# Optimization experiments

Hardware: AMD Instinct MI355X
Metric: run time of the kernel (lower is better)

The kernel has to match this reference:

```python
import jax, jax.numpy as jnp
import numpy as np

B, T, D, H, E = 4, 512, 2048, 1024, 2


def setup_inputs() -> dict:
    key = jax.random.key(0)
    k = jax.random.split(key, 4)
    return {
        "x": jax.random.normal(k[0], (B, T, D), jnp.float32),
        "Wg": jax.random.normal(k[1], (D, E), jnp.float32) / np.float32(np.sqrt(D)),
        "W1": jax.random.normal(k[2], (E, D, H), jnp.float32) / np.float32(np.sqrt(D)),
        "b1": jnp.zeros((E, H), jnp.float32),
        "W2": jax.random.normal(k[3], (E, H, D), jnp.float32) / np.float32(np.sqrt(H)),
        "b2": jnp.zeros((E, D), jnp.float32),
    }


def reference(x, Wg, W1, b1, W2, b2):
    # --- Top1 gate: bias-free linear -> softmax -> argmax routing ---
    logits = jnp.einsum('btd,de->bte', x, Wg)            # [B,T,E]
    probs = jax.nn.softmax(logits, axis=-1)
    idx = jnp.argmax(probs, axis=-1)                     # [B,T] chosen expert
    gate = jnp.max(probs, axis=-1)                       # [B,T] top-1 prob
    # --- expert FFN (identity activation): fc1 -> fc2, batched per expert ---
    h = jnp.einsum('btd,edh->ebth', x, W1) + b1[:, None, None, :]   # [E,B,T,H]
    y = jnp.einsum('ebth,ehd->ebtd', h, W2) + b2[:, None, None, :]  # [E,B,T,D]
    # --- combine: select routed expert output, scale by gate value ---
    sel = jax.nn.one_hot(idx, E, dtype=x.dtype) * gate[..., None]   # [B,T,E]
    moe_out = jnp.einsum('ebtd,bte->btd', y, sel)                   # [B,T,D]
    # --- model head: sum over model_dim, log_softmax over tokens ---
    return jax.nn.log_softmax(jnp.sum(moe_out, axis=2), axis=1)     # [B,T]
```

## Files before the change

### kernel.cpp

```cpp
#include <hip/hip_runtime.h>

#define B_ 4
#define T_ 512
#define D_ 2048
#define H_ 1024
#define E_ 2

__device__ __forceinline__ float waveReduceSum(float v) {
    #pragma unroll
    for (int o = 32; o > 0; o >>= 1) v += __shfl_down(v, o, 64);
    return v;
}

__device__ __forceinline__ float blockReduceSum256(float v, float* lds) {
    int lane = threadIdx.x & 63;
    int wid  = threadIdx.x >> 6;
    v = waveReduceSum(v);
    if (lane == 0) lds[wid] = v;
    __syncthreads();
    float r = 0.f;
    if (threadIdx.x == 0) {
        r = lds[0] + lds[1] + lds[2] + lds[3];
    }
    __syncthreads();
    return r;
}

__global__ void k_w2sum(const float* __restrict__ W2, float* __restrict__ w2s) {
    __shared__ float lds[4];
    int row = blockIdx.x;
    const float* p = W2 + (size_t)row * D_;
    float acc = 0.f;
    for (int i = threadIdx.x * 4; i < D_; i += blockDim.x * 4) {
        float4 v = *reinterpret_cast<const float4*>(p + i);
        acc += (v.x + v.y) + (v.z + v.w);
    }
    acc = blockReduceSum256(acc, lds);
    if (threadIdx.x == 0) w2s[row] = acc;
}

__global__ void k_vred(const float* __restrict__ W1, const float* __restrict__ w2s,
                       float* __restrict__ v) {
    __shared__ float lds[4];
    int row = blockIdx.x;
    int e = row / D_;
    const float* p = W1 + (size_t)row * H_;
    const float* w = w2s + e * H_;
    float acc = 0.f;
    for (int i = threadIdx.x * 4; i < H_; i += blockDim.x * 4) {
        float4 a = *reinterpret_cast<const float4*>(p + i);
        float4 b = *reinterpret_cast<const float4*>(w + i);
        acc += a.x * b.x + a.y * b.y + a.z * b.z + a.w * b.w;
    }
    acc = blockReduceSum256(acc, lds);
    if (threadIdx.x == 0) v[row] = acc;
}

__global__ void k_cbias(const float* __restrict__ b1, const float* __restrict__ w2s,
                        const float* __restrict__ b2, float* __restrict__ c) {
    __shared__ float lds[4];
    int e = blockIdx.x;
    float acc = 0.f;
    for (int i = threadIdx.x; i < H_; i += blockDim.x)
        acc += b1[e * H_ + i] * w2s[e * H_ + i];
    for (int i = threadIdx.x; i < D_; i += blockDim.x)
        acc += b2[e * D_ + i];
    acc = blockReduceSum256(acc, lds);
    if (threadIdx.x == 0) c[e] = acc;
}

__global__ void k_token(const float* __restrict__ x, const float* __restrict__ Wg,
                        const float* __restrict__ v, const float* __restrict__ c,
                        float* __restrict__ s) {
    __shared__ float lds[4][4];
    int bt = blockIdx.x;
    const float* xp = x + (size_t)bt * D_;
    float g0 = 0.f, g1 = 0.f, d0 = 0.f, d1 = 0.f;
    for (int i = threadIdx.x * 4; i < D_; i += blockDim.x * 4) {
        float4 xv   = *reinterpret_cast<const float4*>(xp + i);
        float4 v0   = *reinterpret_cast<const float4*>(v + i);
        float4 v1   = *reinterpret_cast<const float4*>(v + D_ + i);
        float4 wg01 = *reinterpret_cast<const float4*>(Wg + i * 2);
        float4 wg23 = *reinterpret_cast<const float4*>(Wg + i * 2 + 4);
        g0 += xv.x * wg01.x + xv.y * wg01.z + xv.z * wg23.x + xv.w * wg23.z;
        g1 += xv.x * wg01.y + xv.y * wg01.w + xv.z * wg23.y + xv.w * wg23.w;
        d0 += xv.x * v0.x + xv.y * v0.y + xv.z * v0.z + xv.w * v0.w;
        d1 += xv.x * v1.x + xv.y * v1.y + xv.z * v1.z + xv.w * v1.w;
    }
    #pragma unroll
    for (int o = 32; o > 0; o >>= 1) {
        g0 += __shfl_down(g0, o, 64);
        g1 += __shfl_down(g1, o, 64);
        d0 += __shfl_down(d0, o, 64);
        d1 += __shfl_down(d1, o, 64);
    }
    int lane = threadIdx.x & 63;
    int wid  = threadIdx.x >> 6;
    if (lane == 0) {
        lds[wid][0] = g0; lds[wid][1] = g1; lds[wid][2] = d0; lds[wid][3] = d1;
    }
    __syncthreads();
    if (threadIdx.x == 0) {
        float G0 = 0.f, G1 = 0.f, Dt0 = 0.f, Dt1 = 0.f;
        #pragma unroll
        for (int w = 0; w < 4; ++w) {
            G0 += lds[w][0]; G1 += lds[w][1]; Dt0 += lds[w][2]; Dt1 += lds[w][3];
        }
        int e = (G1 > G0) ? 1 : 0;
        float m  = fmaxf(G0, G1);
        float p0 = expf(G0 - m), p1 = expf(G1 - m);
        float gate = ((e == 0) ? p0 : p1) / (p0 + p1);
        float dot  = (e == 0) ? Dt0 : Dt1;
        s[bt] = gate * (dot + c[e]);
    }
}

__global__ void k_lsm(const float* __restrict__ s, float* __restrict__ out) {
    __shared__ float lds[8];
    int b = blockIdx.x;
    int t = threadIdx.x;
    int lane = t & 63, wid = t >> 6;
    float val = s[b * T_ + t];

    float m = val;
    #pragma unroll
    for (int o = 1; o < 64; o <<= 1) m = fmaxf(m, __shfl_xor(m, o, 64));
    if (lane == 0) lds[wid] = m;
    __syncthreads();
    m = lds[0];
    #pragma unroll
    for (int w = 1; w < 8; ++w) m = fmaxf(m, lds[w]);
    __syncthreads();

    float ex = expf(val - m);
    float sum = ex;
    #pragma unroll
    for (int o = 1; o < 64; o <<= 1) sum += __shfl_xor(sum, o, 64);
    if (lane == 0) lds[wid] = sum;
    __syncthreads();
    sum = 0.f;
    #pragma unroll
    for (int w = 0; w < 8; ++w) sum += lds[w];

    out[b * T_ + t] = val - m - logf(sum);
}

extern "C" void kernel_launch(void* const* d_in, const int* in_sizes, int n_in,
                              void* d_out, int out_size, void* d_ws, size_t ws_size,
                              hipStream_t stream) {
    (void)in_sizes; (void)n_in; (void)out_size; (void)ws_size;
    const float* x  = (const float*)d_in[0];
    const float* Wg = (const float*)d_in[1];
    const float* W1 = (const float*)d_in[2];
    const float* b1 = (const float*)d_in[3];
    const float* W2 = (const float*)d_in[4];
    const float* b2 = (const float*)d_in[5];
    float* out = (float*)d_out;

    float* ws  = (float*)d_ws;
    float* w2s = ws;
    float* v   = ws + 2048;
    float* c   = ws + 6144;
    float* s   = ws + 6160;

    k_w2sum<<<E_ * H_, 256, 0, stream>>>(W2, w2s);
    k_vred <<<E_ * D_, 256, 0, stream>>>(W1, w2s, v);
    k_cbias<<<E_,      256, 0, stream>>>(b1, w2s, b2, c);
    k_token<<<B_ * T_, 256, 0, stream>>>(x, Wg, v, c, s);
    k_lsm  <<<B_,      512, 0, stream>>>(s, out);
}
```

Measured before the change: 26.71 us.

## Fuse bias and log-softmax kernels, use one wave per row reductions

Each reduction kernel now assigns a whole row to a single 64-lane wave with fully unrolled float4 loads, so the block-level LDS reductions and barriers go away. The bias-constant computation is folded into the v-reduction kernel as two extra blocks. The final log-softmax is folded into the token kernel through an atomic last-block counter, which is reset in the prep kernel. This cuts the launch count from five to three, at the cost of an atomic and threadfences per block and a serial tail in the last block.

```diff
diff --git a/kernel.cpp b/kernel.cpp
--- a/kernel.cpp
+++ b/kernel.cpp
@@ -1,4 +1,5 @@
 #include <hip/hip_runtime.h>
+#include <math.h>
 
 #define B_ 4
 #define T_ 512
@@ -6,84 +7,86 @@
 #define H_ 1024
 #define E_ 2
 
+#define LD4(p) (*reinterpret_cast<const float4*>(p))
+
 __device__ __forceinline__ float waveReduceSum(float v) {
     #pragma unroll
     for (int o = 32; o > 0; o >>= 1) v += __shfl_down(v, o, 64);
     return v;
 }
 
-__device__ __forceinline__ float blockReduceSum256(float v, float* lds) {
+__global__ __launch_bounds__(256) void k_prep(const float* __restrict__ W2,
+                                              float* __restrict__ w2s,
+                                              int* __restrict__ counter) {
+    if (blockIdx.x == 0 && threadIdx.x == 0) *counter = 0;
+    int gw   = (blockIdx.x * 256 + threadIdx.x) >> 6;
     int lane = threadIdx.x & 63;
-    int wid  = threadIdx.x >> 6;
-    v = waveReduceSum(v);
-    if (lane == 0) lds[wid] = v;
-    __syncthreads();
-    float r = 0.f;
-    if (threadIdx.x == 0) {
-        r = lds[0] + lds[1] + lds[2] + lds[3];
+    const float* p = W2 + (size_t)gw * D_;
+    float acc = 0.f;
+    #pragma unroll
+    for (int k = 0; k < D_ / 256; ++k) {
+        float4 a = LD4(p + (lane + k * 64) * 4);
+        acc += (a.x + a.y) + (a.z + a.w);
     }
-    __syncthreads();
-    return r;
+    acc = waveReduceSum(acc);
+    if (lane == 0) w2s[gw] = acc;
 }
 
-__global__ void k_w2sum(const float* __restrict__ W2, float* __restrict__ w2s) {
-    __shared__ float lds[4];
-    int row = blockIdx.x;
-    const float* p = W2 + (size_t)row * D_;
-    float acc = 0.f;
-    for (int i = threadIdx.x * 4; i < D_; i += blockDim.x * 4) {
-        float4 v = *reinterpret_cast<const float4*>(p + i);
-        acc += (v.x + v.y) + (v.z + v.w);
+__global__ __launch_bounds__(256) void k_vred(const float* __restrict__ W1,
+                                              const float* __restrict__ w2s,
+                                              const float* __restrict__ b1,
+                                              const float* __restrict__ b2,
+                                              float* __restrict__ v,
+                                              float* __restrict__ c) {
+    if (blockIdx.x >= 1024) {
+        __shared__ float lds[4];
+        int e = blockIdx.x - 1024;
+        float acc = 0.f;
+        for (int i = threadIdx.x; i < H_; i += 256) acc += b1[e * H_ + i] * w2s[e * H_ + i];
+        for (int i = threadIdx.x; i < D_; i += 256) acc += b2[e * D_ + i];
+        acc = waveReduceSum(acc);
+        if ((threadIdx.x & 63) == 0) lds[threadIdx.x >> 6] = acc;
+        __syncthreads();
+        if (threadIdx.x == 0) c[e] = lds[0] + lds[1] + lds[2] + lds[3];
+        return;
     }
-    acc = blockReduceSum256(acc, lds);
-    if (threadIdx.x == 0) w2s[row] = acc;
-}
-
-__global__ void k_vred(const float* __restrict__ W1, const float* __restrict__ w2s,
-                       float* __restrict__ v) {
-    __shared__ float lds[4];
-    int row = blockIdx.x;
-    int e = row / D_;
+    int row  = (blockIdx.x * 256 + threadIdx.x) >> 6;
+    int lane = threadIdx.x & 63;
+    int e    = row >> 11;
     const float* p = W1 + (size_t)row * H_;
     const float* w = w2s + e * H_;
     float acc = 0.f;
-    for (int i = threadIdx.x * 4; i < H_; i += blockDim.x * 4) {
-        float4 a = *reinterpret_cast<const float4*>(p + i);
-        float4 b = *reinterpret_cast<const float4*>(w + i);
+    #pragma unroll
+    for (int k = 0; k < H_ / 256; ++k) {
+        float4 a = LD4(p + (lane + k * 64) * 4);
+        float4 b = LD4(w + (lane + k * 64) * 4);
         acc += a.x * b.x + a.y * b.y + a.z * b.z + a.w * b.w;
     }
-    acc = blockReduceSum256(acc, lds);
-    if (threadIdx.x == 0) v[row] = acc;
+    acc = waveReduceSum(acc);
+    if (lane == 0) v[row] = acc;
 }
 
-__global__ void k_cbias(const float* __restrict__ b1, const float* __restrict__ w2s,
-                        const float* __restrict__ b2, float* __restrict__ c) {
-    __shared__ float lds[4];
-    int e = blockIdx.x;
-    float acc = 0.f;
-    for (int i = threadIdx.x; i < H_; i += blockDim.x)
-        acc += b1[e * H_ + i] * w2s[e * H_ + i];
-    for (int i = threadIdx.x; i < D_; i += blockDim.x)
-        acc += b2[e * D_ + i];
-    acc = blockReduceSum256(acc, lds);
-    if (threadIdx.x == 0) c[e] = acc;
-}
-
-__global__ void k_token(const float* __restrict__ x, const float* __restrict__ Wg,
-                        const float* __restrict__ v, const float* __restrict__ c,
-                        float* __restrict__ s) {
-    __shared__ float lds[4][4];
-    int bt = blockIdx.x;
+__global__ __launch_bounds__(256) void k_token(const float* __restrict__ x,
+                                               const float* __restrict__ Wg,
+                                               const float* __restrict__ v,
+                                               const float* __restrict__ c,
+                                               float* __restrict__ s,
+                                               float* __restrict__ out,
+                                               int* __restrict__ counter) {
+    int lane = threadIdx.x & 63;
+    int bt   = (blockIdx.x * 256 + threadIdx.x) >> 6;
     const float* xp = x + (size_t)bt * D_;
     float g0 = 0.f, g1 = 0.f, d0 = 0.f, d1 = 0.f;
-    for (int i = threadIdx.x * 4; i < D_; i += blockDim.x * 4) {
-        float4 xv   = *reinterpret_cast<const float4*>(xp + i);
-        float4 v0   = *reinterpret_cast<const float4*>(v + i);
-        float4 v1   = *reinterpret_cast<const float4*>(v + D_ + i);
-        float4 wg01 = *reinterpret_cast<const float4*>(Wg + i * 2);
-        float4 wg23 = *reinterpret_cast<const float4*>(Wg + i * 2 + 4);
-        g0 += xv.x * wg01.x + xv.y * wg01.z + xv.z * wg23.x + xv.w * wg23.z;
-        g1 += xv.x * wg01.y + xv.y * wg01.w + xv.z * wg23.y + xv.w * wg23.w;
+    #pragma unroll
+    for (int k = 0; k < D_ / 256; ++k) {
+        int i = (lane + k * 64) * 4;
+        float4 xv = LD4(xp + i);
+        float4 v0 = LD4(v + i);
+        float4 v1 = LD4(v + D_ + i);
+        float4 wa = LD4(Wg + 2 * i);
+        float4 wb = LD4(Wg + 2 * i + 4);
+        g0 += xv.x * wa.x + xv.y * wa.z + xv.z * wb.x + xv.w * wb.z;
+        g1 += xv.x * wa.y + xv.y * wa.w + xv.z * wb.y + xv.w * wb.w;
         d0 += xv.x * v0.x + xv.y * v0.y + xv.z * v0.z + xv.w * v0.w;
         d1 += xv.x * v1.x + xv.y * v1.y + xv.z * v1.z + xv.w * v1.w;
     }
@@ -94,55 +97,43 @@
         d0 += __shfl_down(d0, o, 64);
         d1 += __shfl_down(d1, o, 64);
     }
-    int lane = threadIdx.x & 63;
-    int wid  = threadIdx.x >> 6;
     if (lane == 0) {
-        lds[wid][0] = g0; lds[wid][1] = g1; lds[wid][2] = d0; lds[wid][3] = d1;
+        int e = (g1 > g0) ? 1 : 0;
+        float m = fmaxf(g0, g1);
+        float p0 = expf(g0 - m), p1 = expf(g1 - m);
+        float gate = ((e == 0) ? p0 : p1) / (p0 + p1);
+        float dot = (e == 0) ? d0 : d1;
+        s[bt] = gate * (dot + c[e]);
+        __threadfence();
     }
     __syncthreads();
+    __shared__ int isLast;
     if (threadIdx.x == 0) {
-        float G0 = 0.f, G1 = 0.f, Dt0 = 0.f, Dt1 = 0.f;
-        #pragma unroll
-        for (int w = 0; w < 4; ++w) {
-            G0 += lds[w][0]; G1 += lds[w][1]; Dt0 += lds[w][2]; Dt1 += lds[w][3];
-        }
-        int e = (G1 > G0) ? 1 : 0;
-        float m  = fmaxf(G0, G1);
-        float p0 = expf(G0 - m), p1 = expf(G1 - m);
-        float gate = ((e == 0) ? p0 : p1) / (p0 + p1);
-        float dot  = (e == 0) ? Dt0 : Dt1;
-        s[bt] = gate * (dot + c[e]);
+        int old = atomicAdd(counter, 1);
+        isLast = (old == (int)gridDim.x - 1) ? 1 : 0;
     }
-}
-
-__global__ void k_lsm(const float* __restrict__ s, float* __restrict__ out) {
-    __shared__ float lds[8];
-    int b = blockIdx.x;
-    int t = threadIdx.x;
-    int lane = t & 63, wid = t >> 6;
-    float val = s[b * T_ + t];
-
-    float m = val;
+    __syncthreads();
+    if (!isLast) return;
+    __threadfence();
+    int b = threadIdx.x >> 6;
+    const float* sb = s + b * T_;
+    float vals[T_ / 64];
+    float m = -INFINITY;
+    #pragma unroll
+    for (int k = 0; k < T_ / 64; ++k) {
+        vals[k] = sb[lane + k * 64];
+        m = fmaxf(m, vals[k]);
+    }
     #pragma unroll
     for (int o = 1; o < 64; o <<= 1) m = fmaxf(m, __shfl_xor(m, o, 64));
-    if (lane == 0) lds[wid] = m;
-    __syncthreads();
-    m = lds[0];
+    float sum = 0.f;
     #pragma unroll
-    for (int w = 1; w < 8; ++w) m = fmaxf(m, lds[w]);
-    __syncthreads();
-
-    float ex = expf(val - m);
-    float sum = ex;
+    for (int k = 0; k < T_ / 64; ++k) sum += expf(vals[k] - m);
     #pragma unroll
     for (int o = 1; o < 64; o <<= 1) sum += __shfl_xor(sum, o, 64);
-    if (lane == 0) lds[wid] = sum;
-    __syncthreads();
-    sum = 0.f;
+    float lse = m + logf(sum);
     #pragma unroll
-    for (int w = 0; w < 8; ++w) sum += lds[w];
-
-    out[b * T_ + t] = val - m - logf(sum);
+    for (int k = 0; k < T_ / 64; ++k) out[b * T_ + lane + k * 64] = vals[k] - lse;
 }
 
 extern "C" void kernel_launch(void* const* d_in, const int* in_sizes, int n_in,
@@ -157,15 +148,14 @@
     const float* b2 = (const float*)d_in[5];
     float* out = (float*)d_out;
 
-    float* ws  = (float*)d_ws;
-    float* w2s = ws;
-    float* v   = ws + 2048;
-    float* c   = ws + 6144;
-    float* s   = ws + 6160;
+    float* ws   = (float*)d_ws;
+    float* w2s  = ws;
+    float* v    = ws + 2048;
+    float* c    = ws + 6144;
+    int*   ctr  = (int*)(ws + 6148);
+    float* s    = ws + 6160;
 
-    k_w2sum<<<E_ * H_, 256, 0, stream>>>(W2, w2s);
-    k_vred <<<E_ * D_, 256, 0, stream>>>(W1, w2s, v);
-    k_cbias<<<E_,      256, 0, stream>>>(b1, w2s, b2, c);
-    k_token<<<B_ * T_, 256, 0, stream>>>(x, Wg, v, c, s);
-    k_lsm  <<<B_,      512, 0, stream>>>(s, out);
+    k_prep <<<512,  256, 0, stream>>>(W2, w2s, ctr);
+    k_vred <<<1026, 256, 0, stream>>>(W1, w2s, b1, b2, v, c);
+    k_token<<<512,  256, 0, stream>>>(x, Wg, v, c, s, out, ctr);
 }
```

Result: slower. 55.69 us (+108.5%).
